# Kernel optimization log

Hardware: AMD Instinct MI355X
Metric: run time of the kernel (lower is better)

## Reference

```python
import jax, jax.numpy as jnp
import numpy as np

HEADS = 8

def setup_inputs() -> dict:
    key = jax.random.key(0)
    ks = jax.random.split(key, 4)
    b, n, d = 4, 4097, 128  # n = 64*64 + 1 (CLS + spatial)
    x = jax.random.normal(ks[0], (b, n, d), dtype=jnp.float32)
    W_qkv = jax.random.normal(ks[1], (d, 3 * d), dtype=jnp.float32) * (d ** -0.5)
    b_qkv = jnp.zeros((3 * d,), dtype=jnp.float32)
    W_out = jax.random.normal(ks[2], (d, d), dtype=jnp.float32) * (d ** -0.5)
    b_out = jnp.zeros((d,), dtype=jnp.float32)
    return {"x": x, "W_qkv": W_qkv, "b_qkv": b_qkv, "W_out": W_out, "b_out": b_out}

def reference(x, W_qkv, b_qkv, W_out, b_out):
    b, n, d = x.shape
    h = HEADS
    dh = d // h
    scale = d ** -0.5  # note: module scales by dim**-0.5, not head_dim**-0.5
    qkv = x @ W_qkv + b_qkv                      # [b, n, 3d]
    q, k, v = jnp.split(qkv, 3, axis=-1)
    def to_heads(t):
        return t.reshape(b, n, h, dh).transpose(0, 2, 1, 3)  # [b, h, n, dh]
    q, k, v = to_heads(q), to_heads(k), to_heads(v)
    dots = jnp.einsum('bhid,bhjd->bhij', q, k) * scale       # [b, h, n, n]
    attn = jax.nn.softmax(dots, axis=-1)
    out = jnp.einsum('bhij,bhjd->bhid', attn, v)             # [b, h, n, dh]
    out = out.transpose(0, 2, 1, 3).reshape(b, n, d)
    return out @ W_out + b_out
```

## Files before the change

kernel.cpp:

```cpp
#include <hip/hip_runtime.h>
#include <hip/hip_bf16.h>
#include <stdint.h>


#define BB 4
#define NN 4097
#define NNP 4112
#define DD 128
#define HH 8
#define DH 16
#define BH (BB*HH)
#define ROWS (BB*NN)
#define MT  1025
#define NSP 2

typedef _Float16 h4 __attribute__((ext_vector_type(4)));
typedef _Float16 h8 __attribute__((ext_vector_type(8)));
typedef __fp16   fp16v2 __attribute__((ext_vector_type(2)));
typedef float    f4 __attribute__((ext_vector_type(4)));

#define QSCALE (0.08838834764831845f * 1.4426950408889634f)

#if __has_builtin(__builtin_amdgcn_exp2f)
#define EXP2F(x) __builtin_amdgcn_exp2f(x)
#else
#define EXP2F(x) exp2f(x)
#endif

union H4u { h4 v; fp16v2 p[2]; };
union H8u { h8 v; fp16v2 p[4]; };

static __device__ __forceinline__ H4u pack4u(float a, float b, float c, float d) {
    H4u u;
#if __has_builtin(__builtin_amdgcn_cvt_pkrtz)
    u.p[0] = __builtin_amdgcn_cvt_pkrtz(a, b);
    u.p[1] = __builtin_amdgcn_cvt_pkrtz(c, d);
#else
    u.v[0] = (_Float16)a; u.v[1] = (_Float16)b; u.v[2] = (_Float16)c; u.v[3] = (_Float16)d;
#endif
    return u;
}

__global__ __launch_bounds__(256) void prep(
    const float* __restrict__ x,
    const float* __restrict__ Wqkv,
    const float* __restrict__ Wout,
    _Float16* __restrict__ x16,
    _Float16* __restrict__ WqkvT,
    _Float16* __restrict__ WoutT)
{
    const int id = blockIdx.x*256 + threadIdx.x;
    const int NX8 = ROWS*DD/8;
    if (id < NX8) {
        const float4* s = (const float4*)(x + (size_t)id*8);
        const float4 a = s[0], b = s[1];
        const H4u u0 = pack4u(a.x, a.y, a.z, a.w);
        const H4u u1 = pack4u(b.x, b.y, b.z, b.w);
        h4* d = (h4*)(x16 + (size_t)id*8);
        d[0] = u0.v; d[1] = u1.v;
    } else if (id < NX8 + 384*128) {
        const int e = id - NX8;
        const int n = e >> 7, k = e & 127;
        const float s = (n < 128) ? QSCALE : 1.0f;
        WqkvT[e] = (_Float16)(Wqkv[k*384 + n] * s);
    } else if (id < NX8 + 384*128 + 128*128) {
        const int e = id - NX8 - 384*128;
        const int n = e >> 7, k = e & 127;
        WoutT[e] = (_Float16)(Wout[k*128 + n]);
    }
}

__global__ __launch_bounds__(256) void qkv_mfma(
    const _Float16* __restrict__ x16,
    const _Float16* __restrict__ WqkvT,
    const float* __restrict__ bqkv,
    _Float16* __restrict__ Qh,
    _Float16* __restrict__ Kh,
    _Float16* __restrict__ Vh)
{
    const int wid  = blockIdx.x;
    const int wave = threadIdx.x >> 6;
    const int lane = threadIdx.x & 63;
    const int quad = lane >> 4, l16 = lane & 15;

    const int arow = wid*16 + l16;
    const int arc  = (arow < ROWS) ? arow : (ROWS - 1);
    h8 af[4];
    #pragma unroll
    for (int kk = 0; kk < 4; ++kk)
        af[kk] = *(const h8*)(x16 + (size_t)arc*DD + kk*32 + quad*8);

    const int r0 = wid*16 + quad*4;
    const int nt0 = wave*6;

    for (int nt = nt0; nt < nt0 + 6; nt += 2) {
        const float b0 = bqkv[nt*16 + l16]      * ((nt   < 8) ? QSCALE : 1.0f);
        const float b1 = bqkv[nt*16 + 16 + l16] * ((nt+1 < 8) ? QSCALE : 1.0f);
        f4 a0 = {b0,b0,b0,b0}, a1 = {b1,b1,b1,b1};
        #pragma unroll
        for (int kk = 0; kk < 4; ++kk) {
            const h8 bf0 = *(const h8*)(WqkvT + (size_t)(nt*16      + l16)*DD + kk*32 + quad*8);
            const h8 bf1 = *(const h8*)(WqkvT + (size_t)(nt*16 + 16 + l16)*DD + kk*32 + quad*8);
            a0 = __builtin_amdgcn_mfma_f32_16x16x32_f16(af[kk], bf0, a0, 0, 0, 0);
            a1 = __builtin_amdgcn_mfma_f32_16x16x32_f16(af[kk], bf1, a1, 0, 0, 0);
        }
        #pragma unroll
        for (int u = 0; u < 2; ++u) {
            const int ntc = nt + u;
            const int which = ntc >> 3, head = ntc & 7;
            _Float16* base = (which == 0) ? Qh : ((which == 1) ? Kh : Vh);
            const f4 av = u ? a1 : a0;
            #pragma unroll
            for (int r = 0; r < 4; ++r) {
                const int row = r0 + r;
                if (row < ROWS) {
                    const int bidx = row / NN;
                    const int nrow = row - bidx*NN;
                    base[((size_t)(bidx*HH + head)*NNP + nrow)*DH + l16] = (_Float16)av[r];
                }
            }
        }
    }
}

__global__ __launch_bounds__(256) void vt_transpose(
    const _Float16* __restrict__ Vh,
    _Float16* __restrict__ Vt)
{
    __shared__ _Float16 tile[128][DH + 2];
    const int tl  = blockIdx.x;
    const int bh  = blockIdx.y;
    const int tid = threadIdx.x;
    const int n0  = tl * 128;
    const int rem = (n0 + 128 <= NNP) ? 128 : (NNP - n0);

    {
        const int r  = tid >> 1;
        const int i8 = (tid & 1) * 8;
        const int rc = (r < rem) ? r : (rem - 1);
        const h8 v = *(const h8*)(Vh + ((size_t)bh*NNP + n0 + rc)*DH + i8);
        #pragma unroll
        for (int j = 0; j < 8; ++j) tile[r][i8 + j] = v[j];
    }
    __syncthreads();
    {
        const int i    = tid >> 4;
        const int nseg = tid & 15;
        if (nseg * 8 < rem) {
            h8 v;
            #pragma unroll
            for (int j = 0; j < 8; ++j) v[j] = tile[nseg*8 + j][i];
            *(h8*)(Vt + ((size_t)bh*DH + i)*NNP + n0 + nseg*8) = v;
        }
    }
}

__global__ __launch_bounds__(256, 8) void attn_mfma(
    const _Float16* __restrict__ Qh,
    const _Float16* __restrict__ Kh,
    const _Float16* __restrict__ Vt,
    _Float16* __restrict__ PACC,
    float* __restrict__ PL)
{
    const int qt   = blockIdx.x;
    const int bh   = blockIdx.y;
    const int sp   = blockIdx.z;
    const int tid  = threadIdx.x;
    const int wave = tid >> 6;
    const int lane = tid & 63;
    const int quad = lane >> 4;
    const int l16  = lane & 15;
    const int bidx = bh >> 3, head = bh & 7;

    const int qbase = qt*256 + wave*64;

    const _Float16* Qb = Qh + (size_t)bh*NNP*DH;
    h4 qf[4];
    #pragma unroll
    for (int g = 0; g < 4; ++g) {
        const int qr = qbase + g*16 + l16;
        const int qc = (qr < NN) ? qr : (NN-1);
        qf[g] = *(const h4*)(Qb + (size_t)qc*DH + quad*4);
    }

    f4 acc[4] = {{0,0,0,0},{0,0,0,0},{0,0,0,0},{0,0,0,0}};
    float ls[4] = {0.f,0.f,0.f,0.f};

    const int t0 = sp*(4096/NSP/16);
    const int t1 = t0 + (4096/NSP/16);

    const _Float16* kp = Kh + ((size_t)bh*NNP + (size_t)t0*16 + l16)*DH + quad*4;
    const _Float16* vp = Vt + ((size_t)bh*DH + l16)*NNP + t0*16 + quad*4;

    h4 ak = *(const h4*)kp;
    h4 av = *(const h4*)vp;
    const f4 zero = {0.f,0.f,0.f,0.f};
#if __has_builtin(__builtin_amdgcn_fdot2)
    const fp16v2 one2 = {(__fp16)1.0f, (__fp16)1.0f};
#endif

    #pragma unroll 2
    for (int tt = t0; tt < t1; ++tt) {
        kp += 16*DH; vp += 16;
        const h4 nak = *(const h4*)kp;
        const h4 nav = *(const h4*)vp;
        #pragma unroll
        for (int g = 0; g < 4; ++g) {
            f4 d = __builtin_amdgcn_mfma_f32_16x16x16f16(ak, qf[g], zero, 0, 0, 0);
            const float p0 = EXP2F(d[0]), p1 = EXP2F(d[1]), p2 = EXP2F(d[2]), p3 = EXP2F(d[3]);
            const H4u pb = pack4u(p0, p1, p2, p3);
#if __has_builtin(__builtin_amdgcn_fdot2)
            ls[g] = __builtin_amdgcn_fdot2(pb.p[0], one2,
                     __builtin_amdgcn_fdot2(pb.p[1], one2, ls[g], false), false);
#else
            ls[g] += (p0 + p1) + (p2 + p3);
#endif
            acc[g] = __builtin_amdgcn_mfma_f32_16x16x16f16(av, pb.v, acc[g], 0, 0, 0);
        }
        ak = nak; av = nav;
    }

    if (sp == NSP-1) {
        #pragma unroll
        for (int g = 0; g < 4; ++g) {
            f4 d = __builtin_amdgcn_mfma_f32_16x16x16f16(ak, qf[g], zero, 0, 0, 0);
            const float p0 = (quad == 0) ? EXP2F(d[0]) : 0.f;
            ls[g] += p0;
            const H4u pb = pack4u(p0, 0.f, 0.f, 0.f);
            acc[g] = __builtin_amdgcn_mfma_f32_16x16x16f16(av, pb.v, acc[g], 0, 0, 0);
        }
    }

    const size_t rb = (size_t)sp*ROWS + (size_t)bidx*NN;
    #pragma unroll
    for (int g = 0; g < 4; ++g) {
        float l = ls[g];
        l += __shfl_xor(l, 16);
        l += __shfl_xor(l, 32);
        const int qr = qbase + g*16 + l16;
        if (qr < NN) {
            const float inv = 1.0f / l;
            const H4u st = pack4u(acc[g][0]*inv, acc[g][1]*inv, acc[g][2]*inv, acc[g][3]*inv);
            *(h4*)(PACC + (rb + qr)*DD + head*DH + quad*4) = st.v;
            if (quad == 0) PL[(rb + qr)*HH + head] = l;
        }
    }
}

__global__ __launch_bounds__(256, 1) void out_mfma(
    const _Float16* __restrict__ PACC,
    const float* __restrict__ PL,
    const _Float16* __restrict__ WoutT,
    const float* __restrict__ bout,
    float* __restrict__ out)
{
    const int wid  = blockIdx.x*4 + (threadIdx.x >> 6);
    if (wid >= MT) return;
    const int lane = threadIdx.x & 63;
    const int quad = lane >> 4, l16 = lane & 15;
    const int hq   = quad >> 1;

    const int arow = wid*16 + l16;
    const int arc  = (arow < ROWS) ? arow : (ROWS - 1);

    h8 pf[NSP][4]; float lv[NSP][4];
    #pragma unroll
    for (int sp = 0; sp < NSP; ++sp) {
        const _Float16* pb  = PACC + ((size_t)sp*ROWS + arc)*DD;
        const float*    plb = PL   + ((size_t)sp*ROWS + arc)*HH;
        #pragma unroll
        for (int kk = 0; kk < 4; ++kk) {
            pf[sp][kk] = *(const h8*)(pb + kk*32 + quad*8);
            lv[sp][kk] = plb[kk*2 + hq];
        }
    }
    h8 wf[4][2][4];
    #pragma unroll
    for (int p = 0; p < 4; ++p)
        #pragma unroll
        for (int u = 0; u < 2; ++u)
            #pragma unroll
            for (int kk = 0; kk < 4; ++kk)
                wf[p][u][kk] = *(const h8*)(WoutT + (size_t)((p*2+u)*16 + l16)*DD + kk*32 + quad*8);

    h8 af[4];
    #pragma unroll
    for (int kk = 0; kk < 4; ++kk) {
        const float l0 = lv[0][kk], l1 = lv[1][kk];
        const float inv = 1.0f / (l0 + l1);
        const float s0 = l0*inv, s1 = l1*inv;
        H8u u;
        #pragma unroll
        for (int j = 0; j < 4; ++j) {
            const float a = s0*(float)pf[0][kk][2*j]   + s1*(float)pf[1][kk][2*j];
            const float b = s0*(float)pf[0][kk][2*j+1] + s1*(float)pf[1][kk][2*j+1];
#if __has_builtin(__builtin_amdgcn_cvt_pkrtz)
            u.p[j] = __builtin_amdgcn_cvt_pkrtz(a, b);
#else
            u.v[2*j] = (_Float16)a; u.v[2*j+1] = (_Float16)b;
#endif
        }
        af[kk] = u.v;
    }

    const int r0 = wid*16 + quad*4;

    #pragma unroll
    for (int p = 0; p < 4; ++p) {
        const int nt = p*2;
        const float b0 = bout[nt*16 + l16];
        const float b1 = bout[nt*16 + 16 + l16];
        f4 a0 = {b0,b0,b0,b0}, a1 = {b1,b1,b1,b1};
        #pragma unroll
        for (int kk = 0; kk < 4; ++kk) {
            a0 = __builtin_amdgcn_mfma_f32_16x16x32_f16(af[kk], wf[p][0][kk], a0, 0, 0, 0);
            a1 = __builtin_amdgcn_mfma_f32_16x16x32_f16(af[kk], wf[p][1][kk], a1, 0, 0, 0);
        }
        #pragma unroll
        for (int r = 0; r < 4; ++r) {
            const int row = r0 + r;
            if (row < ROWS) {
                out[(size_t)row*DD + nt*16      + l16] = a0[r];
                out[(size_t)row*DD + nt*16 + 16 + l16] = a1[r];
            }
        }
    }
}

extern "C" void kernel_launch(void* const* d_in, const int* in_sizes, int n_in,
                              void* d_out, int out_size, void* d_ws, size_t ws_size,
                              hipStream_t stream) {
    const float* x    = (const float*)d_in[0];
    const float* Wqkv = (const float*)d_in[1];
    const float* bqkv = (const float*)d_in[2];
    const float* Wout = (const float*)d_in[3];
    const float* bout = (const float*)d_in[4];
    for (int i = 0; i < n_in; ++i) {
        switch (in_sizes[i]) {
            case 2097664: x    = (const float*)d_in[i]; break;
            case 49152:   Wqkv = (const float*)d_in[i]; break;
            case 384:     bqkv = (const float*)d_in[i]; break;
            case 16384:   Wout = (const float*)d_in[i]; break;
            case 128:     bout = (const float*)d_in[i]; break;
            default: break;
        }
    }
    float* out = (float*)d_out;

    const size_t perh = (size_t)BH * NNP * DH;
    _Float16* Qh   = (_Float16*)d_ws;
    _Float16* Kh   = Qh + perh;
    _Float16* Vt   = Kh + perh;
    _Float16* Vh   = Vt + perh;
    _Float16* PACC = Vh;
    _Float16* x16  = Vh + perh;
    float*    PL    = (float*)(PACC + (size_t)NSP*ROWS*DD);
    _Float16* WqkvT = (_Float16*)(PL + (size_t)NSP*ROWS*HH);
    _Float16* WoutT = WqkvT + 384*128;

    const int NX8 = ROWS*DD/8;
    const int prep_total = NX8 + 384*128 + 128*128;

    hipLaunchKernelGGL(prep, dim3((prep_total + 255)/256), dim3(256), 0, stream,
                       x, Wqkv, Wout, x16, WqkvT, WoutT);
    hipLaunchKernelGGL(qkv_mfma, dim3(MT), dim3(256), 0, stream,
                       x16, WqkvT, bqkv, Qh, Kh, Vh);
    hipLaunchKernelGGL(vt_transpose, dim3(33, BH), dim3(256), 0, stream,
                       Vh, Vt);
    hipLaunchKernelGGL(attn_mfma, dim3(17, BH, NSP), dim3(256), 0, stream,
                       Qh, Kh, Vt, PACC, PL);
    hipLaunchKernelGGL(out_mfma, dim3((MT + 3)/4), dim3(256), 0, stream,
                       PACC, PL, WoutT, bout, out);
}
```

Measured before the change: 185.3 us.

## Split attention keys four ways and fuse the x fp16 cast into QKV

The key dimension of attention is now split into four parts instead of two, doubling the number of attention blocks to fill the GPU better. The out-projection combine is generalised to sum and renormalise over all splits. The fp32-to-fp16 conversion of x moves from the prep kernel into the QKV GEMM, which saves one full write and re-read of x. QKV outputs are staged in shared memory so each row goes to global memory as vectorized 16-element stores. The cost is a larger partial-result buffer with more combine traffic, and the loop unroll pragma is dropped.

```diff
diff --git a/kernel.cpp b/kernel.cpp
--- a/kernel.cpp
+++ b/kernel.cpp
@@ -12,7 +12,7 @@
 #define BH (BB*HH)
 #define ROWS (BB*NN)
 #define MT  1025
-#define NSP 2
+#define NSP 4
 
 typedef _Float16 h4 __attribute__((ext_vector_type(4)));
 typedef _Float16 h8 __attribute__((ext_vector_type(8)));
@@ -41,43 +41,47 @@
     return u;
 }
 
+static __device__ __forceinline__ h8 pack8u(const float4& t0, const float4& t1) {
+    H8u u;
+#if __has_builtin(__builtin_amdgcn_cvt_pkrtz)
+    u.p[0] = __builtin_amdgcn_cvt_pkrtz(t0.x, t0.y);
+    u.p[1] = __builtin_amdgcn_cvt_pkrtz(t0.z, t0.w);
+    u.p[2] = __builtin_amdgcn_cvt_pkrtz(t1.x, t1.y);
+    u.p[3] = __builtin_amdgcn_cvt_pkrtz(t1.z, t1.w);
+#else
+    u.v[0]=(_Float16)t0.x; u.v[1]=(_Float16)t0.y; u.v[2]=(_Float16)t0.z; u.v[3]=(_Float16)t0.w;
+    u.v[4]=(_Float16)t1.x; u.v[5]=(_Float16)t1.y; u.v[6]=(_Float16)t1.z; u.v[7]=(_Float16)t1.w;
+#endif
+    return u.v;
+}
+
 __global__ __launch_bounds__(256) void prep(
-    const float* __restrict__ x,
     const float* __restrict__ Wqkv,
     const float* __restrict__ Wout,
-    _Float16* __restrict__ x16,
     _Float16* __restrict__ WqkvT,
     _Float16* __restrict__ WoutT)
 {
     const int id = blockIdx.x*256 + threadIdx.x;
-    const int NX8 = ROWS*DD/8;
-    if (id < NX8) {
-        const float4* s = (const float4*)(x + (size_t)id*8);
-        const float4 a = s[0], b = s[1];
-        const H4u u0 = pack4u(a.x, a.y, a.z, a.w);
-        const H4u u1 = pack4u(b.x, b.y, b.z, b.w);
-        h4* d = (h4*)(x16 + (size_t)id*8);
-        d[0] = u0.v; d[1] = u1.v;
-    } else if (id < NX8 + 384*128) {
-        const int e = id - NX8;
-        const int n = e >> 7, k = e & 127;
+    if (id < 384*128) {
+        const int n = id >> 7, k = id & 127;
         const float s = (n < 128) ? QSCALE : 1.0f;
-        WqkvT[e] = (_Float16)(Wqkv[k*384 + n] * s);
-    } else if (id < NX8 + 384*128 + 128*128) {
-        const int e = id - NX8 - 384*128;
+        WqkvT[id] = (_Float16)(Wqkv[k*384 + n] * s);
+    } else if (id < 384*128 + 128*128) {
+        const int e = id - 384*128;
         const int n = e >> 7, k = e & 127;
         WoutT[e] = (_Float16)(Wout[k*128 + n]);
     }
 }
 
 __global__ __launch_bounds__(256) void qkv_mfma(
-    const _Float16* __restrict__ x16,
+    const float* __restrict__ x,
     const _Float16* __restrict__ WqkvT,
     const float* __restrict__ bqkv,
     _Float16* __restrict__ Qh,
     _Float16* __restrict__ Kh,
     _Float16* __restrict__ Vh)
 {
+    __shared__ _Float16 tile[16][392];
     const int wid  = blockIdx.x;
     const int wave = threadIdx.x >> 6;
     const int lane = threadIdx.x & 63;
@@ -85,12 +89,15 @@
 
     const int arow = wid*16 + l16;
     const int arc  = (arow < ROWS) ? arow : (ROWS - 1);
+    const float* xr = x + (size_t)arc*DD;
     h8 af[4];
     #pragma unroll
-    for (int kk = 0; kk < 4; ++kk)
-        af[kk] = *(const h8*)(x16 + (size_t)arc*DD + kk*32 + quad*8);
-
-    const int r0 = wid*16 + quad*4;
+    for (int kk = 0; kk < 4; ++kk) {
+        const float4 t0 = *(const float4*)(xr + kk*32 + quad*8);
+        const float4 t1 = *(const float4*)(xr + kk*32 + quad*8 + 4);
+        af[kk] = pack8u(t0, t1);
+    }
+
     const int nt0 = wave*6;
 
     for (int nt = nt0; nt < nt0 + 6; nt += 2) {
@@ -107,18 +114,25 @@
         #pragma unroll
         for (int u = 0; u < 2; ++u) {
             const int ntc = nt + u;
+            const f4 av = u ? a1 : a0;
+            #pragma unroll
+            for (int r = 0; r < 4; ++r)
+                tile[quad*4 + r][ntc*16 + l16] = (_Float16)av[r];
+        }
+    }
+    __syncthreads();
+
+    for (int u = threadIdx.x; u < 384; u += 256) {
+        const int ntc = u >> 4, lt = u & 15;
+        const int row = wid*16 + lt;
+        if (row < ROWS) {
             const int which = ntc >> 3, head = ntc & 7;
             _Float16* base = (which == 0) ? Qh : ((which == 1) ? Kh : Vh);
-            const f4 av = u ? a1 : a0;
-            #pragma unroll
-            for (int r = 0; r < 4; ++r) {
-                const int row = r0 + r;
-                if (row < ROWS) {
-                    const int bidx = row / NN;
-                    const int nrow = row - bidx*NN;
-                    base[((size_t)(bidx*HH + head)*NNP + nrow)*DH + l16] = (_Float16)av[r];
-                }
-            }
+            const int bidx = row / NN;
+            const int nrow = row - bidx*NN;
+            _Float16* dst = base + ((size_t)(bidx*HH + head)*NNP + nrow)*DH;
+            *(h8*)dst       = *(const h8*)&tile[lt][ntc*16];
+            *(h8*)(dst + 8) = *(const h8*)&tile[lt][ntc*16 + 8];
         }
     }
 }
@@ -186,8 +200,8 @@
     f4 acc[4] = {{0,0,0,0},{0,0,0,0},{0,0,0,0},{0,0,0,0}};
     float ls[4] = {0.f,0.f,0.f,0.f};
 
-    const int t0 = sp*(4096/NSP/16);
-    const int t1 = t0 + (4096/NSP/16);
+    const int t0 = sp*64;
+    const int t1 = t0 + 64;
 
     const _Float16* kp = Kh + ((size_t)bh*NNP + (size_t)t0*16 + l16)*DH + quad*4;
     const _Float16* vp = Vt + ((size_t)bh*DH + l16)*NNP + t0*16 + quad*4;
@@ -199,7 +213,6 @@
     const fp16v2 one2 = {(__fp16)1.0f, (__fp16)1.0f};
 #endif
 
-    #pragma unroll 2
     for (int tt = t0; tt < t1; ++tt) {
         kp += 16*DH; vp += 16;
         const h4 nak = *(const h4*)kp;
@@ -220,7 +233,7 @@
         ak = nak; av = nav;
     }
 
-    if (sp == NSP-1) {
+    if (sp == 3) {
         #pragma unroll
         for (int g = 0; g < 4; ++g) {
             f4 d = __builtin_amdgcn_mfma_f32_16x16x16f16(ak, qf[g], zero, 0, 0, 0);
@@ -286,14 +299,20 @@
     h8 af[4];
     #pragma unroll
     for (int kk = 0; kk < 4; ++kk) {
-        const float l0 = lv[0][kk], l1 = lv[1][kk];
-        const float inv = 1.0f / (l0 + l1);
-        const float s0 = l0*inv, s1 = l1*inv;
+        float lsum = 0.f;
+        #pragma unroll
+        for (int sp = 0; sp < NSP; ++sp) lsum += lv[sp][kk];
+        const float inv = 1.0f / lsum;
         H8u u;
         #pragma unroll
         for (int j = 0; j < 4; ++j) {
-            const float a = s0*(float)pf[0][kk][2*j]   + s1*(float)pf[1][kk][2*j];
-            const float b = s0*(float)pf[0][kk][2*j+1] + s1*(float)pf[1][kk][2*j+1];
+            float a = 0.f, b = 0.f;
+            #pragma unroll
+            for (int sp = 0; sp < NSP; ++sp) {
+                const float s = lv[sp][kk]*inv;
+                a += s*(float)pf[sp][kk][2*j];
+                b += s*(float)pf[sp][kk][2*j+1];
+            }
 #if __has_builtin(__builtin_amdgcn_cvt_pkrtz)
             u.p[j] = __builtin_amdgcn_cvt_pkrtz(a, b);
 #else
@@ -353,18 +372,16 @@
     _Float16* Vt   = Kh + perh;
     _Float16* Vh   = Vt + perh;
     _Float16* PACC = Vh;
-    _Float16* x16  = Vh + perh;
     float*    PL    = (float*)(PACC + (size_t)NSP*ROWS*DD);
     _Float16* WqkvT = (_Float16*)(PL + (size_t)NSP*ROWS*HH);
     _Float16* WoutT = WqkvT + 384*128;
 
-    const int NX8 = ROWS*DD/8;
-    const int prep_total = NX8 + 384*128 + 128*128;
+    const int prep_total = 384*128 + 128*128;
 
     hipLaunchKernelGGL(prep, dim3((prep_total + 255)/256), dim3(256), 0, stream,
-                       x, Wqkv, Wout, x16, WqkvT, WoutT);
+                       Wqkv, Wout, WqkvT, WoutT);
     hipLaunchKernelGGL(qkv_mfma, dim3(MT), dim3(256), 0, stream,
-                       x16, WqkvT, bqkv, Qh, Kh, Vh);
+                       x, WqkvT, bqkv, Qh, Kh, Vh);
     hipLaunchKernelGGL(vt_transpose, dim3(33, BH), dim3(256), 0, stream,
                        Vh, Vt);
     hipLaunchKernelGGL(attn_mfma, dim3(17, BH, NSP), dim3(256), 0, stream,
```

Measured after the change: 179.4 us. -3.2%, faster.
